# Performance work log

Measured on AMD Instinct MI355X. Metric: run time of the kernel, lower is better.

The kernel has to match this reference:

```python
import jax, jax.numpy as jnp
import numpy as np


def setup_inputs() -> dict:
    key = jax.random.key(0)
    k1, k2 = jax.random.split(key)
    B, C, H, W = 8, 21, 512, 512
    inp = jax.random.normal(k1, (B, C, H, W), dtype=jnp.float32)
    target = jax.random.randint(k2, (B, H, W), 0, C, dtype=jnp.int64)
    return {"input": inp, "target": target}


def reference(input, target):
    # input: (B, C, H, W) logits; target: (B, H, W) int labels in [0, C)
    B, C, H, W = input.shape
    N = H * W
    logits = input.reshape(B, C, N)                      # (B, C, N)
    tgt = target.reshape(B, N)                           # (B, N)
    tgt_f = tgt.astype(logits.dtype)

    probs = jax.nn.softmax(logits, axis=1)               # (B, C, N)
    # foreground mask per class: (B, C, N)
    fg = (tgt[:, None, :] == jnp.arange(C)[None, :, None]).astype(logits.dtype)
    errors = jnp.abs(fg - probs)                         # (B, C, N)

    # descending sort along N, vectorized over all (B, C) rows
    perm = jnp.argsort(-errors, axis=2)                  # (B, C, N)
    errors_sorted = jnp.take_along_axis(errors, perm, axis=2)
    # faithful to kornia: gather the raw float labels (not the binary mask)
    tgt_bc = jnp.broadcast_to(tgt_f[:, None, :], (B, C, N))
    target_sorted = jnp.take_along_axis(tgt_bc, perm, axis=2)  # (B, C, N)

    tsum = jnp.sum(target_sorted, axis=2, keepdims=True)       # (B, C, 1)
    intersection = tsum - jnp.cumsum(target_sorted, axis=2)
    union = tsum + jnp.cumsum(1.0 - target_sorted, axis=2)
    gradient = 1.0 - intersection / union                      # (B, C, N)
    # in-place diff along last axis: g[..., 1:] -= g[..., :-1]
    gradient = jnp.concatenate(
        [gradient[..., :1], gradient[..., 1:] - gradient[..., :-1]], axis=-1
    )

    # per-class loss = mean over batch of sum over pixels; final = mean over classes
    loss_bc = jnp.sum(jax.nn.relu(errors_sorted) * gradient, axis=2)  # (B, C)
    return jnp.mean(loss_bc)
```

## Files before the change

### kernel.cpp

```cpp
#include <hip/hip_runtime.h>


#define NB    8
#define NC    21
#define NPIX  262144
#define NROWS (NB * NC)
#define NBINS 2048
#define NB1   1928

__global__ __launch_bounds__(256) void k_err(
    const float* __restrict__ x,
    const int* __restrict__ tgt,
    unsigned short* __restrict__ pk) {
  int t4 = blockIdx.x * blockDim.x + threadIdx.x;
  int b  = t4 >> 16;
  int n4 = (t4 & 65535) << 2;

  const float* xp = x + (size_t)b * NC * NPIX + n4;

  float v[NC][4];
  float m[4] = {-3.4e38f, -3.4e38f, -3.4e38f, -3.4e38f};
  #pragma unroll
  for (int c = 0; c < NC; ++c) {
    float4 t = *(const float4*)(xp + (size_t)c * NPIX);
    v[c][0] = t.x; v[c][1] = t.y; v[c][2] = t.z; v[c][3] = t.w;
    m[0] = fmaxf(m[0], t.x); m[1] = fmaxf(m[1], t.y);
    m[2] = fmaxf(m[2], t.z); m[3] = fmaxf(m[3], t.w);
  }
  float Z[4] = {0.f, 0.f, 0.f, 0.f};
  #pragma unroll
  for (int c = 0; c < NC; ++c) {
    #pragma unroll
    for (int j = 0; j < 4; ++j) {
      v[c][j] = __expf(v[c][j] - m[j]);
      Z[j] += v[c][j];
    }
  }
  float iZ[4];
  #pragma unroll
  for (int j = 0; j < 4; ++j) iZ[j] = 1.0f / Z[j];

  int4 tv = *(const int4*)(tgt + (size_t)b * NPIX + n4);
  int tl[4] = {tv.x, tv.y, tv.z, tv.w};

  unsigned short* op = pk + (size_t)b * NC * NPIX + n4;
  #pragma unroll
  for (int c = 0; c < NC; ++c) {
    ushort4 st;
    unsigned short* sp = (unsigned short*)&st;
    #pragma unroll
    for (int j = 0; j < 4; ++j) {
      float p = v[c][j] * iZ[j];
      float e = fabsf(((c == tl[j]) ? 1.0f : 0.0f) - p);
      unsigned fb   = __float_as_uint(e);
      int      fexp = (int)(fb >> 23) - 127;
      unsigned key  = (fexp < -14) ? 0u
                    : (((unsigned)(fexp + 15) << 7) | ((fb >> 16) & 127u));
      if (key > 1920u) key = 1920u;
      sp[j] = (unsigned short)((key << 5) | (unsigned)tl[j]);
    }
    *(ushort4*)(op + (size_t)c * NPIX) = st;
  }
}

__device__ inline unsigned long long shfl_up_u64(unsigned long long v, int off) {
  unsigned lo = (unsigned)v, hi = (unsigned)(v >> 32);
  lo = (unsigned)__shfl_up((int)lo, off, 64);
  hi = (unsigned)__shfl_up((int)hi, off, 64);
  return ((unsigned long long)hi << 32) | lo;
}
__device__ inline unsigned long long shfl_down_u64(unsigned long long v, int off) {
  unsigned lo = (unsigned)v, hi = (unsigned)(v >> 32);
  lo = (unsigned)__shfl_down((int)lo, off, 64);
  hi = (unsigned)__shfl_down((int)hi, off, 64);
  return ((unsigned long long)hi << 32) | lo;
}

__global__ __launch_bounds__(1024) void k_hist_scan(
    const unsigned short* __restrict__ pk,
    float* __restrict__ out) {
  int row  = blockIdx.x;
  int tid  = threadIdx.x;
  int lane = tid & 63;
  int wave = tid >> 6;

  __shared__ unsigned long long hist0[NBINS];
  __shared__ unsigned long long hist1[3][NB1];
  __shared__ unsigned long long wtot[16];
  __shared__ double wred[16];
  __shared__ double sT;

  for (int i = tid; i < NBINS; i += 1024) hist0[i] = 0;
  for (int i = tid; i < 3 * NB1; i += 1024) ((unsigned long long*)hist1)[i] = 0;
  __syncthreads();

  int rep = wave >> 2;
  unsigned long long* hr = (rep == 0) ? hist0 : hist1[rep - 1];

  const uint4* rp = (const uint4*)(pk + (size_t)row * NPIX);
  #pragma unroll 2
  for (int it = 0; it < 32; ++it) {
    uint4 q = rp[it * 1024 + tid];
    unsigned w[4] = {q.x, q.y, q.z, q.w};
    #pragma unroll
    for (int k = 0; k < 4; ++k) {
      unsigned p0 = w[k] & 0xffffu, p1 = w[k] >> 16;
      atomicAdd(hr + (p0 >> 5), (1ULL << 32) | (unsigned long long)(p0 & 31u));
      atomicAdd(hr + (p1 >> 5), (1ULL << 32) | (unsigned long long)(p1 & 31u));
    }
  }
  __syncthreads();

  unsigned long long tot = 0;
  for (int i = tid; i < NBINS; i += 1024) {
    unsigned long long s = hist0[i];
    if (i < NB1) s += hist1[0][i] + hist1[1][i] + hist1[2][i];
    hist0[i] = s;
    tot += s;
  }
  __syncthreads();

  #pragma unroll
  for (int off = 32; off > 0; off >>= 1) tot += shfl_down_u64(tot, off);
  if (lane == 0) wtot[wave] = tot;
  __syncthreads();
  if (tid == 0) {
    unsigned long long g = 0;
    #pragma unroll
    for (int w = 0; w < 16; ++w) g += wtot[w];
    sT = (double)(unsigned)(g & 0xffffffffULL);
  }
  __syncthreads();
  double T = sT;
  __syncthreads();

  unsigned long long run = 0;
  double acc = 0.0;
  for (int iter = 0; iter < 2; ++iter) {
    int d   = iter * 1024 + tid;
    int bin = (NBINS - 1) - d;
    unsigned long long v = hist0[bin];

    unsigned long long s = v;
    #pragma unroll
    for (int off = 1; off < 64; off <<= 1) {
      unsigned long long u = shfl_up_u64(s, off);
      if (lane >= off) s += u;
    }
    if (lane == 63) wtot[wave] = s;
    __syncthreads();

    unsigned long long woff = 0;
    for (int w = 0; w < wave; ++w) woff += wtot[w];
    unsigned long long excl = s - v + woff + run;

    unsigned n = (unsigned)(v >> 32);
    if (n) {
      unsigned sl = (unsigned)(v & 0xffffffffu);
      unsigned cb = (unsigned)(excl >> 32);
      unsigned sb = (unsigned)(excl & 0xffffffffu);
      double Sb = (double)sb + (double)sl;
      double gb = 1.0 - (T - Sb) / (T + (double)(cb + n) - Sb);
      double ga = (cb == 0) ? 0.0
                            : 1.0 - (T - (double)sb) / (T + (double)cb - (double)sb);
      unsigned key = (unsigned)bin;
      unsigned ex5 = key >> 7, mant = key & 127u;
      float e = (ex5 == 0) ? 0.0f
              : ldexpf(1.0f + ((float)mant + 0.5f) * 0.0078125f, (int)ex5 - 15);
      acc += (double)e * (gb - ga);
    }

    unsigned long long ct = 0;
    #pragma unroll
    for (int w = 0; w < 16; ++w) ct += wtot[w];
    run += ct;
    __syncthreads();
  }

  #pragma unroll
  for (int off = 32; off > 0; off >>= 1) acc += __shfl_down(acc, off, 64);
  if (lane == 0) wred[wave] = acc;
  __syncthreads();
  if (tid == 0) {
    double ssum = 0.0;
    #pragma unroll
    for (int w = 0; w < 16; ++w) ssum += wred[w];
    atomicAdd(out, (float)(ssum * (1.0 / (double)NROWS)));
  }
}

extern "C" void kernel_launch(void* const* d_in, const int* in_sizes, int n_in,
                              void* d_out, int out_size, void* d_ws, size_t ws_size,
                              hipStream_t stream) {
  const float* x  = (const float*)d_in[0];
  const int* tgt  = (const int*)d_in[1];
  float* out      = (float*)d_out;
  unsigned short* pk = (unsigned short*)d_ws;

  hipMemsetAsync(d_out, 0, sizeof(float), stream);

  int quads = NB * NPIX / 4;
  k_err<<<quads / 256, 256, 0, stream>>>(x, tgt, pk);
  k_hist_scan<<<NROWS, 1024, 0, stream>>>(pk, out);
}
```

Before: 294.1 us.

## Split per-row histogram into many partial-row blocks with packed 32-bit LDS atomics

Splits the histogram build, previously one 1024-thread block per row, into 32 blocks of 256 threads per row. Each block writes a partial histogram to workspace, and a separate scan kernel sums the partials before the existing prefix scan and loss accumulation. The LDS atomics also shrink from 64-bit to 32-bit, packing the count in the upper 14 bits and the label sum in the lower 18. The aim is to fill the GPU better (168 blocks was too few) and to make the shared-memory atomics cheaper, at the cost of an extra launch and about 44 MB of partial-histogram traffic through global memory.

```diff
diff --git a/kernel.cpp b/kernel.cpp
--- a/kernel.cpp
+++ b/kernel.cpp
@@ -1,12 +1,13 @@
 #include <hip/hip_runtime.h>
 
 
-#define NB    8
-#define NC    21
-#define NPIX  262144
-#define NROWS (NB * NC)
-#define NBINS 2048
-#define NB1   1928
+#define NB     8
+#define NC     21
+#define NPIX   262144
+#define NROWS  (NB * NC)
+#define NBINS  2048
+#define NPARTS 32
+#define PPP    (NPIX / NPARTS)
 
 __global__ __launch_bounds__(256) void k_err(
     const float* __restrict__ x,
@@ -63,6 +64,40 @@
   }
 }
 
+__global__ __launch_bounds__(256) void k_hist(
+    const unsigned short* __restrict__ pk,
+    unsigned* __restrict__ partial) {
+  int blk  = blockIdx.x;
+  int row  = blk >> 5;
+  int part = blk & 31;
+  int tid  = threadIdx.x;
+  int wave = tid >> 6;
+
+  __shared__ unsigned hist[4][NBINS];
+  #pragma unroll
+  for (int i = tid; i < 4 * NBINS; i += 256) ((unsigned*)hist)[i] = 0;
+  __syncthreads();
+
+  unsigned* hr = hist[wave];
+  const uint4* rp = (const uint4*)(pk + (size_t)row * NPIX + (size_t)part * PPP);
+  #pragma unroll
+  for (int it = 0; it < 4; ++it) {
+    uint4 q = rp[it * 256 + tid];
+    unsigned w[4] = {q.x, q.y, q.z, q.w};
+    #pragma unroll
+    for (int k = 0; k < 4; ++k) {
+      unsigned p0 = w[k] & 0xffffu, p1 = w[k] >> 16;
+      atomicAdd(hr + (p0 >> 5), (1u << 18) | (p0 & 31u));
+      atomicAdd(hr + (p1 >> 5), (1u << 18) | (p1 & 31u));
+    }
+  }
+  __syncthreads();
+
+  unsigned* op = partial + (size_t)blk * NBINS;
+  for (int i = tid; i < NBINS; i += 256)
+    op[i] = hist[0][i] + hist[1][i] + hist[2][i] + hist[3][i];
+}
+
 __device__ inline unsigned long long shfl_up_u64(unsigned long long v, int off) {
   unsigned lo = (unsigned)v, hi = (unsigned)(v >> 32);
   lo = (unsigned)__shfl_up((int)lo, off, 64);
@@ -76,8 +111,8 @@
   return ((unsigned long long)hi << 32) | lo;
 }
 
-__global__ __launch_bounds__(1024) void k_hist_scan(
-    const unsigned short* __restrict__ pk,
+__global__ __launch_bounds__(1024) void k_scan(
+    const unsigned* __restrict__ partial,
     float* __restrict__ out) {
   int row  = blockIdx.x;
   int tid  = threadIdx.x;
@@ -85,41 +120,26 @@
   int wave = tid >> 6;
 
   __shared__ unsigned long long hist0[NBINS];
-  __shared__ unsigned long long hist1[3][NB1];
   __shared__ unsigned long long wtot[16];
   __shared__ double wred[16];
   __shared__ double sT;
 
-  for (int i = tid; i < NBINS; i += 1024) hist0[i] = 0;
-  for (int i = tid; i < 3 * NB1; i += 1024) ((unsigned long long*)hist1)[i] = 0;
-  __syncthreads();
-
-  int rep = wave >> 2;
-  unsigned long long* hr = (rep == 0) ? hist0 : hist1[rep - 1];
-
-  const uint4* rp = (const uint4*)(pk + (size_t)row * NPIX);
-  #pragma unroll 2
-  for (int it = 0; it < 32; ++it) {
-    uint4 q = rp[it * 1024 + tid];
-    unsigned w[4] = {q.x, q.y, q.z, q.w};
-    #pragma unroll
-    for (int k = 0; k < 4; ++k) {
-      unsigned p0 = w[k] & 0xffffu, p1 = w[k] >> 16;
-      atomicAdd(hr + (p0 >> 5), (1ULL << 32) | (unsigned long long)(p0 & 31u));
-      atomicAdd(hr + (p1 >> 5), (1ULL << 32) | (unsigned long long)(p1 & 31u));
-    }
+  #pragma unroll
+  for (int bp = 0; bp < 2; ++bp) {
+    int bn = bp * 1024 + tid;
+    const unsigned* pp = partial + (size_t)row * NPARTS * NBINS + bn;
+    unsigned long long s = 0;
+    #pragma unroll
+    for (int p = 0; p < NPARTS; ++p) {
+      unsigned v = pp[(size_t)p * NBINS];
+      s += ((unsigned long long)(v >> 18) << 32) | (unsigned long long)(v & 0x3FFFFu);
+    }
+    hist0[bn] = s;
   }
   __syncthreads();
 
   unsigned long long tot = 0;
-  for (int i = tid; i < NBINS; i += 1024) {
-    unsigned long long s = hist0[i];
-    if (i < NB1) s += hist1[0][i] + hist1[1][i] + hist1[2][i];
-    hist0[i] = s;
-    tot += s;
-  }
-  __syncthreads();
-
+  for (int i = tid; i < NBINS; i += 1024) tot += hist0[i];
   #pragma unroll
   for (int off = 32; off > 0; off >>= 1) tot += shfl_down_u64(tot, off);
   if (lane == 0) wtot[wave] = tot;
@@ -136,6 +156,7 @@
 
   unsigned long long run = 0;
   double acc = 0.0;
+  #pragma unroll
   for (int iter = 0; iter < 2; ++iter) {
     int d   = iter * 1024 + tid;
     int bin = (NBINS - 1) - d;
@@ -195,11 +216,14 @@
   const float* x  = (const float*)d_in[0];
   const int* tgt  = (const int*)d_in[1];
   float* out      = (float*)d_out;
+
   unsigned short* pk = (unsigned short*)d_ws;
+  unsigned* partial  = (unsigned*)((char*)d_ws + (size_t)NROWS * NPIX * 2);
 
   hipMemsetAsync(d_out, 0, sizeof(float), stream);
 
   int quads = NB * NPIX / 4;
   k_err<<<quads / 256, 256, 0, stream>>>(x, tgt, pk);
-  k_hist_scan<<<NROWS, 1024, 0, stream>>>(pk, out);
-}
+  k_hist<<<NROWS * NPARTS, 256, 0, stream>>>(pk, partial);
+  k_scan<<<NROWS, 1024, 0, stream>>>(partial, out);
+}
```

New measurement: 306.6 us. 1.04x slower.
